# Kernel tuning notes

Hardware: AMD Instinct MI355X
Metric: run time of the kernel (lower is better)

The kernel has to match this reference:

```python
import jax, jax.numpy as jnp
import numpy as np

K_MASK = -2.3819763e+38

B, T, D = 2, 2048, 2048
N_HEADS, N_KV, HEAD_DIM = 16, 8, 128
SCALAR = 0.08838834764831845  # head_dim ** -0.5
ROPE_BASE = 10000


def rms_norm(x, scale):
    # fp32 mean-of-squares, rsqrt, bf16 round-trip, then scale (as in QwemmaRMSNorm)
    x32 = x.astype(jnp.float32)
    var = jnp.mean(jnp.square(x32), axis=-1, keepdims=True)
    rescaled = (x32 * jax.lax.rsqrt(var + 1e-06)).astype(jnp.bfloat16)
    return rescaled * scale


def apply_rope(inputs, positions, base_frequency):
    head_dim = inputs.shape[-1]
    fraction = 2 * jnp.arange(0, head_dim // 2) / head_dim
    timescale = base_frequency ** fraction
    sinusoid = positions[..., jnp.newaxis] / timescale[jnp.newaxis, jnp.newaxis, :]
    sinusoid = sinusoid[..., jnp.newaxis, :]  # [B,T,1,H/2]
    sin = jnp.sin(sinusoid).astype(inputs.dtype)
    cos = jnp.cos(sinusoid).astype(inputs.dtype)
    first, second = jnp.split(inputs, 2, axis=-1)
    out = jnp.concatenate([first * cos - second * sin,
                           second * cos + first * sin], axis=-1)
    return out.astype(inputs.dtype)


def setup_inputs() -> dict:
    key = jax.random.key(0)
    ks = jax.random.split(key, 7)
    x = jax.random.normal(ks[0], (B, T, D), dtype=jnp.float32)
    segment_pos = jnp.broadcast_to(jnp.arange(T, dtype=jnp.int32)[None, :], (B, T))
    attn_mask = jnp.broadcast_to(jnp.tril(jnp.ones((T, T), dtype=bool))[None], (B, T, T))
    q_w = jax.random.normal(ks[1], (N_HEADS, D, HEAD_DIM), dtype=jnp.float32) * 0.02
    kv_w = jax.random.normal(ks[2], (2, N_KV, D, HEAD_DIM), dtype=jnp.float32) * 0.02
    o_w = jax.random.normal(ks[3], (N_HEADS, HEAD_DIM, D), dtype=jnp.float32) * 0.02
    q_scale = 1.0 + 0.1 * jax.random.normal(ks[4], (HEAD_DIM,), dtype=jnp.float32)
    k_scale = 1.0 + 0.1 * jax.random.normal(ks[5], (HEAD_DIM,), dtype=jnp.float32)
    return {"x": x, "segment_pos": segment_pos, "attn_mask": attn_mask,
            "q_w": q_w, "kv_w": kv_w, "o_w": o_w,
            "q_scale": q_scale, "k_scale": k_scale}


def reference(x, segment_pos, attn_mask, q_w, kv_w, o_w, q_scale, k_scale):
    # projections
    q = jnp.einsum('BTD,NDH->BTNH', x, q_w)
    k, v = jnp.einsum('BSD,CKDH->CBSKH', x, kv_w)
    # QK RMSNorm + RoPE
    q = apply_rope(rms_norm(q, q_scale), segment_pos, ROPE_BASE)
    k = apply_rope(rms_norm(k, k_scale), segment_pos, ROPE_BASE)
    # GQA: [B,T,N,H] -> [B,T,K,G,H]
    b, t, n, h = q.shape
    g = n // N_KV
    q = q.reshape((b, t, N_KV, g, h))
    logits = jnp.einsum('BTKGH,BSKH->BTKGS', q, k)
    logits = (logits.astype(jnp.float32) * SCALAR).astype(jnp.bfloat16)
    s = logits.shape[-1]
    logits = logits.reshape((b, t, n, s))
    padded = jnp.where(jnp.expand_dims(attn_mask, -2), logits, K_MASK)
    probs = jax.nn.softmax(padded.astype(jnp.float32), axis=-1).astype(k.dtype)
    probs = probs.reshape((b, t, N_KV, g, s))
    encoded = jnp.einsum('BTKGS,BSKH->BTKGH', probs, v)
    encoded = encoded.reshape((b, t, n, h))
    return jnp.einsum('BTNH,NHD->BTD', encoded, o_w)


if __name__ == '__main__':
    out = reference(**setup_inputs())
    print(out.shape, out.dtype)
```

## Files before the change

kernel.cpp:

```cpp
#include <hip/hip_runtime.h>

typedef unsigned short u16;
typedef __attribute__((ext_vector_type(4))) float f32x4;
typedef __attribute__((ext_vector_type(8))) short s16x8;

#define SCALAR_F 0.08838834764831845f
#define KMASKF (-1e30f)

__device__ __forceinline__ u16 f2b(float f){
  unsigned u = __float_as_uint(f);
  unsigned r = u + 0x7FFFu + ((u>>16)&1u);
  return (u16)(r>>16);
}
__device__ __forceinline__ float b2f(u16 h){ return __uint_as_float(((unsigned)h)<<16); }

__device__ __forceinline__ f32x4 mfma16(s16x8 a, s16x8 b, f32x4 c){
  return __builtin_amdgcn_mfma_f32_16x16x32_bf16(a, b, c, 0, 0, 0);
}

__device__ __forceinline__ void glds16(const u16* g, u16* l){
  __builtin_amdgcn_global_load_lds((const __attribute__((address_space(1))) unsigned*)g,
                                   (__attribute__((address_space(3))) unsigned*)l, 16, 0, 0);
}

#define PHASE_BAR() asm volatile("s_barrier" ::: "memory")
#define LGKM0()     do { asm volatile("s_waitcnt lgkmcnt(0)" ::: "memory"); __builtin_amdgcn_sched_barrier(0); } while(0)

__global__ __launch_bounds__(256) void cvt_f32_bf16(const float* __restrict__ in, u16* __restrict__ out){
  int i = blockIdx.x*256 + threadIdx.x;
  const float4* p = (const float4*)in;
  float4 a = p[2*i], b = p[2*i+1];
  s16x8 r;
  r[0]=(short)f2b(a.x); r[1]=(short)f2b(a.y); r[2]=(short)f2b(a.z); r[3]=(short)f2b(a.w);
  r[4]=(short)f2b(b.x); r[5]=(short)f2b(b.y); r[6]=(short)f2b(b.z); r[7]=(short)f2b(b.w);
  *(s16x8*)(out + (size_t)i*8) = r;
}

__global__ __launch_bounds__(256) void build_wqkvt(const float* __restrict__ qw, const float* __restrict__ kvw,
                                                   u16* __restrict__ out){
  __shared__ float t[64][65];
  int head = blockIdx.z;
  int d0 = blockIdx.y*64, h0 = blockIdx.x*64;
  const float* src; int colbase;
  if (head < 16){ src = qw + (size_t)head*2048*128; colbase = head*128; }
  else if (head < 24){ int k = head-16; src = kvw + (size_t)k*2048*128; colbase = 2048 + k*128; }
  else { int k = head-24; src = kvw + (size_t)(8+k)*2048*128; colbase = 3072 + k*128; }
  int tid = threadIdx.x;
  #pragma unroll
  for (int p=0;p<16;p++){ int e = p*256+tid; int r = e>>6, c = e&63;
    t[r][c] = src[(size_t)(d0+r)*128 + h0 + c]; }
  __syncthreads();
  #pragma unroll
  for (int p=0;p<16;p++){ int e = p*256+tid; int c = e>>6, r = e&63;
    out[(size_t)(colbase + h0 + c)*2048 + d0 + r] = f2b(t[r][c]); }
}

__global__ __launch_bounds__(256) void tr2048(const float* __restrict__ src, u16* __restrict__ out){
  __shared__ float t[64][65];
  int r0 = blockIdx.y*64, c0 = blockIdx.x*64;
  int tid = threadIdx.x;
  #pragma unroll
  for (int p=0;p<16;p++){ int e = p*256+tid; int r = e>>6, c = e&63;
    t[r][c] = src[(size_t)(r0+r)*2048 + c0 + c]; }
  __syncthreads();
  #pragma unroll
  for (int p=0;p<16;p++){ int e = p*256+tid; int c = e>>6, r = e&63;
    out[(size_t)(c0+c)*2048 + r0 + r] = f2b(t[r][c]); }
}

__global__ __launch_bounds__(256) void rope_table(float* __restrict__ table){
  int tid = blockIdx.x*256 + threadIdx.x;
  int pos = tid>>6, i = tid&63;
  float ts = powf(10000.f, (float)i * (1.f/64.f));
  float ang = (float)pos / ts;
  ((float2*)table)[tid] = make_float2(sinf(ang), cosf(ang));
}

__global__ __launch_bounds__(512,2) void gemm256(const u16* __restrict__ A, const u16* __restrict__ Bt,
                                                 u16* __restrict__ C, int K, int ldc){
  __shared__ u16 Als[2][2][128*64];
  __shared__ u16 Bls[2][2][128*64];
  const int tid = threadIdx.x;
  const int wid = tid>>6, l = tid&63;
  const int wr = wid>>2, wc = wid&3;
  const int l15 = l&15, lg = l>>4;
  const int wg = blockIdx.x;
  const int swz = (wg&7)*32 + (wg>>3);
  const size_t m0 = (size_t)(swz>>4)*256, n0 = (size_t)(swz&15)*256;

  const f32x4 z4 = {0.f,0.f,0.f,0.f};
  f32x4 acc[8][4];
  #pragma unroll
  for (int mi=0;mi<8;mi++)
    #pragma unroll
    for (int ni=0;ni<4;ni++) acc[mi][ni] = z4;

  auto stageA = [&](int k0, int bi, int h){
    #pragma unroll
    for (int c=0;c<2;c++){
      int g = c*512 + tid;
      int row = g>>3, pg = g&7;
      glds16(A + (m0 + h*128 + row)*K + k0 + ((pg ^ (row&7))<<3), &Als[bi][h][0] + g*8);
    }
  };
  auto stageB = [&](int k0, int bi, int h){
    #pragma unroll
    for (int c=0;c<2;c++){
      int g = c*512 + tid;
      int row = g>>3, pg = g&7;
      glds16(Bt + (n0 + h*128 + row)*K + k0 + ((pg ^ (row&7))<<3), &Bls[bi][h][0] + g*8);
    }
  };

  s16x8 af[8][2], bf[4][2];

  const int NT = K>>6;
  stageA(0,0,0); stageA(0,0,1); stageB(0,0,0); stageB(0,0,1);
  stageA(64,1,0); stageA(64,1,1);
  asm volatile("s_waitcnt vmcnt(4)" ::: "memory");
  PHASE_BAR();

  for (int t=0; t<NT; ++t){
    const int bi = t&1;
    const char* Ab = (const char*)&Als[bi][wr][0];
    const char* Bb = (const char*)&Bls[bi][wc>>1][0];
    const int brl = (wc&1)*64;
    const int kn1 = (t+1)<<6, kn2 = (t+2)<<6;

    #pragma unroll
    for (int mi=0;mi<4;mi++){
      int r = mi*16 + l15;
      #pragma unroll
      for (int kk=0;kk<2;kk++)
        af[mi][kk] = *(const s16x8*)(Ab + r*128 + (((kk*4+lg) ^ (r&7))<<4));
    }
    #pragma unroll
    for (int ni=0;ni<2;ni++){
      int r = brl + ni*16 + l15;
      #pragma unroll
      for (int kk=0;kk<2;kk++)
        bf[ni][kk] = *(const s16x8*)(Bb + r*128 + (((kk*4+lg) ^ (r&7))<<4));
    }
    if (t+1 < NT) stageB(kn1, bi^1, 0);
    PHASE_BAR(); LGKM0();
    __builtin_amdgcn_s_setprio(1);
    #pragma unroll
    for (int mi=0;mi<4;mi++)
      #pragma unroll
      for (int ni=0;ni<2;ni++)
        #pragma unroll
        for (int kk=0;kk<2;kk++)
          acc[mi][ni] = mfma16(af[mi][kk], bf[ni][kk], acc[mi][ni]);
    __builtin_amdgcn_s_setprio(0);
    PHASE_BAR();

    #pragma unroll
    for (int ni=2;ni<4;ni++){
      int r = brl + ni*16 + l15;
      #pragma unroll
      for (int kk=0;kk<2;kk++)
        bf[ni][kk] = *(const s16x8*)(Bb + r*128 + (((kk*4+lg) ^ (r&7))<<4));
    }
    if (t+1 < NT) stageB(kn1, bi^1, 1);
    PHASE_BAR(); LGKM0();
    __builtin_amdgcn_s_setprio(1);
    #pragma unroll
    for (int mi=0;mi<4;mi++)
      #pragma unroll
      for (int ni=2;ni<4;ni++)
        #pragma unroll
        for (int kk=0;kk<2;kk++)
          acc[mi][ni] = mfma16(af[mi][kk], bf[ni][kk], acc[mi][ni]);
    __builtin_amdgcn_s_setprio(0);
    PHASE_BAR();

    #pragma unroll
    for (int mi=4;mi<8;mi++){
      int r = mi*16 + l15;
      #pragma unroll
      for (int kk=0;kk<2;kk++)
        af[mi][kk] = *(const s16x8*)(Ab + r*128 + (((kk*4+lg) ^ (r&7))<<4));
    }
    PHASE_BAR(); LGKM0();
    __builtin_amdgcn_s_setprio(1);
    #pragma unroll
    for (int mi=4;mi<8;mi++)
      #pragma unroll
      for (int ni=2;ni<4;ni++)
        #pragma unroll
        for (int kk=0;kk<2;kk++)
          acc[mi][ni] = mfma16(af[mi][kk], bf[ni][kk], acc[mi][ni]);
    __builtin_amdgcn_s_setprio(0);
    PHASE_BAR();

    if (t+2 < NT){ stageA(kn2, bi, 0); stageA(kn2, bi, 1); }
    __builtin_amdgcn_s_setprio(1);
    #pragma unroll
    for (int mi=4;mi<8;mi++)
      #pragma unroll
      for (int ni=0;ni<2;ni++)
        #pragma unroll
        for (int kk=0;kk<2;kk++)
          acc[mi][ni] = mfma16(af[mi][kk], bf[ni][kk], acc[mi][ni]);
    __builtin_amdgcn_s_setprio(0);
    if (t < NT-2)      { asm volatile("s_waitcnt vmcnt(4)" ::: "memory"); }
    else if (t == NT-2){ asm volatile("s_waitcnt vmcnt(0)" ::: "memory"); }
    PHASE_BAR();
  }

  #pragma unroll
  for (int mi=0;mi<8;mi++)
    #pragma unroll
    for (int ni=0;ni<4;ni++)
      #pragma unroll
      for (int r=0;r<4;r++){
        size_t row = m0 + wr*128 + mi*16 + lg*4 + r;
        size_t col = n0 + wc*64 + ni*16 + l15;
        C[row*ldc + col] = f2b(acc[mi][ni][r]);
      }
}

template<bool OUTBF16>
__global__ __launch_bounds__(256) void gemm_bt(const u16* __restrict__ A, const u16* __restrict__ Bt,
                                               void* __restrict__ C, int K, int ldc){
  __shared__ u16 As[128*64];
  __shared__ u16 Bs[128*64];
  const int tid = threadIdx.x, w = tid>>6, l = tid&63;
  const int wm = w>>1, wn = w&1;
  const int l15 = l&15, lg = l>>4, l7 = l&7;
  const size_t m0 = (size_t)blockIdx.y*128, n0 = (size_t)blockIdx.x*128;
  const f32x4 z4 = {0.f,0.f,0.f,0.f};
  f32x4 acc[4][4];
  #pragma unroll
  for (int m=0;m<4;m++)
    #pragma unroll
    for (int n=0;n<4;n++) acc[m][n] = z4;
  const char* AsB = (const char*)As; const char* BsB = (const char*)Bs;
  int colsw[2];
  colsw[0] = (lg*16) ^ (l7<<4);
  colsw[1] = (64 + lg*16) ^ (l7<<4);
  int arow[4], brow[4];
  #pragma unroll
  for (int m=0;m<4;m++){ arow[m] = (wm*64 + m*16 + l15)*128; brow[m] = (wn*64 + m*16 + l15)*128; }
  const int sgl = l7 ^ (l>>3);
  for (int k0=0;k0<K;k0+=64){
    #pragma unroll
    for (int i=0;i<4;i++){
      int slot = (w*4+i)*64 + l;
      int row = slot>>3;
      glds16(A  + (m0+row)*K + k0 + sgl*8, (u16*)As + slot*8);
      glds16(Bt + (n0+row)*K + k0 + sgl*8, (u16*)Bs + slot*8);
    }
    __syncthreads();
    #pragma unroll
    for (int kb=0;kb<2;kb++){
      s16x8 af[4], bf[4];
      #pragma unroll
      for (int m=0;m<4;m++) af[m] = *(const s16x8*)(AsB + arow[m] + colsw[kb]);
      #pragma unroll
      for (int n=0;n<4;n++) bf[n] = *(const s16x8*)(BsB + brow[n] + colsw[kb]);
      #pragma unroll
      for (int m=0;m<4;m++)
        #pragma unroll
        for (int n=0;n<4;n++)
          acc[m][n] = mfma16(af[m], bf[n], acc[m][n]);
    }
    __syncthreads();
  }
  #pragma unroll
  for (int m=0;m<4;m++)
    #pragma unroll
    for (int n=0;n<4;n++)
      #pragma unroll
      for (int r=0;r<4;r++){
        size_t row = m0 + wm*64 + m*16 + lg*4 + r;
        size_t col = n0 + wn*64 + n*16 + l15;
        if (OUTBF16) ((u16*)C)[row*ldc + col] = f2b(acc[m][n][r]);
        else ((float*)C)[row*ldc + col] = acc[m][n][r];
      }
}

__global__ __launch_bounds__(256) void norm_rope(const u16* __restrict__ qkv, const float* __restrict__ table,
                                                 const float* __restrict__ scale, const int* __restrict__ segpos,
                                                 u16* __restrict__ dst, int nhl2, int colbase, float mult){
  int w = threadIdx.x>>6, l = threadIdx.x&63;
  int rid = blockIdx.x*4 + w;
  int bt = rid >> nhl2;
  int n  = rid & ((1<<nhl2)-1);
  int b = bt >> 11, t = bt & 2047;
  const u16* src = qkv + (size_t)bt*4096 + colbase + n*128;
  float x1 = b2f(src[l]), x2 = b2f(src[64+l]);
  float ss = x1*x1 + x2*x2;
  #pragma unroll
  for (int off=32; off; off>>=1) ss += __shfl_xor(ss, off);
  float rs = rsqrtf(ss*(1.f/128.f) + 1e-6f);
  float v1 = x1*rs*scale[l], v2 = x2*rs*scale[64+l];
  int pos = segpos[bt];
  float2 sc = ((const float2*)table)[pos*64 + l];
  float o1 = (v1*sc.y - v2*sc.x)*mult;
  float o2 = (v2*sc.y + v1*sc.x)*mult;
  u16* d = dst + (((size_t)((b<<nhl2) + n))*2048 + t)*128;
  d[l] = f2b(o1); d[64+l] = f2b(o2);
}

__global__ __launch_bounds__(256) void vtr(const u16* __restrict__ qkv, u16* __restrict__ vt){
  __shared__ float t[64][65];
  int bk = blockIdx.z;
  int t0 = blockIdx.y*64, d0 = blockIdx.x*64;
  int b = bk>>3, kv = bk&7;
  int tid = threadIdx.x;
  #pragma unroll
  for (int p=0;p<16;p++){ int e = p*256+tid; int r = e>>6, c = e&63;
    t[r][c] = b2f(qkv[(size_t)(b*2048 + t0 + r)*4096 + 3072 + kv*128 + d0 + c]); }
  __syncthreads();
  #pragma unroll
  for (int p=0;p<16;p++){ int e = p*256+tid; int c = e>>6, r = e&63;
    vt[((size_t)bk*128 + d0 + c)*2048 + t0 + r] = f2b(t[r][c]); }
}

__global__ __launch_bounds__(256,2) void attn_kern(const u16* __restrict__ qn, const u16* __restrict__ kn,
                                                   const u16* __restrict__ vt, u16* __restrict__ enc){
  __shared__ u16 Ks[2][64*128];
  __shared__ u16 Vs[2][64*128];
  __shared__ u16 Ps[4*16*64];
  const int idx = blockIdx.x;
  const int pp = idx>>5;
  const int hb = idx & 31;
  const int hn = hb & 15, b = hb >> 4;
  const int kv = hn>>1;
  const int tid = threadIdx.x, w = tid>>6, l = tid&63;
  const int l15 = l&15, lg = l>>4;
  const u16* qh = qn + ((size_t)(b*16+hn))*2048*128;
  const u16* kh = kn + ((size_t)(b*8+kv))*2048*128;
  const u16* vh = vt + ((size_t)(b*8+kv))*128*2048;
  const int qbA = pp, qbB = 31-pp;

  int qr0 = qbA*64 + w*16;
  s16x8 qf[4];
  #pragma unroll
  for (int kb=0;kb<4;kb++)
    qf[kb] = *(const s16x8*)(qh + (size_t)(qr0 + l15)*128 + kb*32 + lg*8);

  const f32x4 z4 = {0.f,0.f,0.f,0.f};
  f32x4 o[8];
  #pragma unroll
  for (int dn=0;dn<8;dn++) o[dn] = z4;
  float mrow[4], lp[4];
  #pragma unroll
  for (int r=0;r<4;r++){ mrow[r] = KMASKF; lp[r] = 0.f; }

  const char* KsB0 = (const char*)&Ks[0][0];
  const char* VsB0 = (const char*)&Vs[0][0];
  char* PsB = (char*)Ps + w*2048;

  auto stage = [&](int s0, int bi){
    #pragma unroll
    for (int i=0;i<4;i++){
      int slot = (w*4+i)*64 + l;
      { int row = slot>>4, g = slot&15, gl = g ^ (row&7);
        glds16(kh + (size_t)(s0+row)*128 + gl*8, &Ks[bi][0] + slot*8); }
      { int row = slot>>3, g = slot&7, gl = g ^ (row&7);
        glds16(vh + (size_t)row*2048 + s0 + gl*8, &Vs[bi][0] + slot*8); }
    }
  };

  auto epilogue = [&](int qr){
    #pragma unroll
    for (int r=0;r<4;r++){
      float s = lp[r];
      s += __shfl_xor(s,1); s += __shfl_xor(s,2); s += __shfl_xor(s,4); s += __shfl_xor(s,8);
      lp[r] = 1.f/s;
    }
    #pragma unroll
    for (int dn=0;dn<8;dn++)
      #pragma unroll
      for (int r=0;r<4;r++){
        size_t row = (size_t)b*2048 + qr + lg*4 + r;
        size_t col = hn*128 + dn*16 + l15;
        enc[row*2048 + col] = f2b(o[dn][r]*lp[r]);
      }
  };

  stage(0, 0);
  __syncthreads();

  int cur = 0;
  for (int it=0; it<=32; ++it){
    if (it < 32){
      int s0n = (it+1 <= pp) ? (it+1)*64 : (it-pp)*64;
      stage(s0n, cur^1);
    }
    const int s0 = (it <= pp) ? it*64 : (it-pp-1)*64;
    const char* KsB = KsB0 + cur*16384;
    const char* VsB = VsB0 + cur*16384;

    f32x4 sa[4];
    #pragma unroll
    for (int nc=0;nc<4;nc++) sa[nc] = z4;
    #pragma unroll
    for (int kb=0;kb<4;kb++){
      s16x8 kf[4];
      #pragma unroll
      for (int nc=0;nc<4;nc++){
        int srow = nc*16 + l15;
        int cb = (kb*64 + lg*16) ^ ((srow&7)<<4);
        kf[nc] = *(const s16x8*)(KsB + srow*256 + cb);
      }
      #pragma unroll
      for (int nc=0;nc<4;nc++)
        sa[nc] = mfma16(qf[kb], kf[nc], sa[nc]);
    }
    if (it == pp || it == 32){
      #pragma unroll
      for (int nc=0;nc<4;nc++)
        #pragma unroll
        for (int r=0;r<4;r++){
          int row = qr0 + lg*4 + r;
          int col = s0 + nc*16 + l15;
          if (col > row) sa[nc][r] = KMASKF;
        }
    }
    #pragma unroll
    for (int r=0;r<4;r++){
      float pm = fmaxf(fmaxf(sa[0][r], sa[1][r]), fmaxf(sa[2][r], sa[3][r]));
      pm = fmaxf(pm, __shfl_xor(pm,1));
      pm = fmaxf(pm, __shfl_xor(pm,2));
      pm = fmaxf(pm, __shfl_xor(pm,4));
      pm = fmaxf(pm, __shfl_xor(pm,8));
      float mo = mrow[r];
      float mn = fmaxf(mo, pm);
      float sc = __expf(mo - mn);
      mrow[r] = mn;
      int rowp = lg*4 + r;
      float ls = 0.f;
      #pragma unroll
      for (int nc=0;nc<4;nc++){
        float p = __expf(sa[nc][r] - mn);
        ls += p;
        int cb = ((nc*16 + l15)*2) ^ ((rowp&7)<<4);
        *(u16*)(PsB + rowp*128 + cb) = f2b(p);
      }
      lp[r] = lp[r]*sc + ls;
      #pragma unroll
      for (int dn=0;dn<8;dn++) o[dn][r] *= sc;
    }
    asm volatile("" ::: "memory");
    #pragma unroll
    for (int kb=0;kb<2;kb++){
      int rowp = l15;
      int cbp = (kb*64 + lg*16) ^ ((rowp&7)<<4);
      s16x8 pf = *(const s16x8*)(PsB + rowp*128 + cbp);
      #pragma unroll
      for (int dn=0;dn<8;dn++){
        int vrow = dn*16 + l15;
        int cb = (kb*64 + lg*16) ^ ((vrow&7)<<4);
        s16x8 vf = *(const s16x8*)(VsB + vrow*128 + cb);
        o[dn] = mfma16(pf, vf, o[dn]);
      }
    }
    if (it == pp){
      epilogue(qr0);
      qr0 = qbB*64 + w*16;
      #pragma unroll
      for (int kb=0;kb<4;kb++)
        qf[kb] = *(const s16x8*)(qh + (size_t)(qr0 + l15)*128 + kb*32 + lg*8);
      #pragma unroll
      for (int dn=0;dn<8;dn++) o[dn] = z4;
      #pragma unroll
      for (int r=0;r<4;r++){ mrow[r] = KMASKF; lp[r] = 0.f; }
    }
    __syncthreads();
    cur ^= 1;
  }
  epilogue(qr0);
}

extern "C" void kernel_launch(void* const* d_in, const int* in_sizes, int n_in,
                              void* d_out, int out_size, void* d_ws, size_t ws_size,
                              hipStream_t stream){
  const float* x      = (const float*)d_in[0];
  const int*   segpos = (const int*)d_in[1];
  const float* qw     = (const float*)d_in[3];
  const float* kvw    = (const float*)d_in[4];
  const float* ow     = (const float*)d_in[5];
  const float* qs     = (const float*)d_in[6];
  const float* ks     = (const float*)d_in[7];
  float* out = (float*)d_out;

  char* ws = (char*)d_ws;
  size_t off = 0;
  auto alloc = [&](size_t bytes)->void*{ void* p = ws + off; off += (bytes + 255) & ~(size_t)255; return p; };
  u16*   xb    = (u16*)alloc((size_t)4096*2048*2);
  u16*   wqkvt = (u16*)alloc((size_t)4096*2048*2);
  u16*   wot   = (u16*)alloc((size_t)2048*2048*2);
  u16*   qkv   = (u16*)alloc((size_t)4096*4096*2);
  u16*   qn    = (u16*)alloc((size_t)2*16*2048*128*2);
  u16*   kn    = (u16*)alloc((size_t)2*8*2048*128*2);
  u16*   vt    = (u16*)alloc((size_t)2*8*128*2048*2);
  u16*   enc   = (u16*)alloc((size_t)4096*2048*2);
  float* table = (float*)alloc((size_t)2048*64*2*4);

  cvt_f32_bf16<<<4096,256,0,stream>>>(x, xb);
  build_wqkvt<<<dim3(2,32,32),256,0,stream>>>(qw, kvw, wqkvt);
  tr2048<<<dim3(32,32),256,0,stream>>>(ow, wot);
  rope_table<<<512,256,0,stream>>>(table);
  gemm256<<<256,512,0,stream>>>(xb, wqkvt, qkv, 2048, 4096);
  norm_rope<<<16384,256,0,stream>>>(qkv, table, qs, segpos, qn, 4, 0,    SCALAR_F);
  norm_rope<<<8192, 256,0,stream>>>(qkv, table, ks, segpos, kn, 3, 2048, 1.0f);
  vtr<<<dim3(2,32,16),256,0,stream>>>(qkv, vt);
  attn_kern<<<512,256,0,stream>>>(qn, kn, vt, enc);
  gemm_bt<false><<<dim3(16,32),256,0,stream>>>(enc, wot, out, 2048, 2048);
}
```

Before: 358.6 us.

## Pipeline output GEMM, load V from global directly, lazy softmax rescale

Replaces the simple output-projection GEMM with a 512-thread, 256x128-tile kernel. It double-buffers K-tiles through LDS, uses a swizzled block order, splits MFMA phases with priority hints, and hides loads behind vmcnt waits. In attention, V tiles are no longer staged through LDS; each lane reads its V fragments straight from global memory, which frees LDS so occupancy can rise to 3 blocks per CU. The online softmax now skips the rescale unless the running max grows by more than 8 in some lane. This saves exp and multiply work, but uncoalesced global V reads and the looser max bound could cost performance or precision.

```diff
diff --git a/kernel.cpp b/kernel.cpp
--- a/kernel.cpp
+++ b/kernel.cpp
@@ -220,63 +220,135 @@
       }
 }
 
-template<bool OUTBF16>
-__global__ __launch_bounds__(256) void gemm_bt(const u16* __restrict__ A, const u16* __restrict__ Bt,
-                                               void* __restrict__ C, int K, int ldc){
-  __shared__ u16 As[128*64];
-  __shared__ u16 Bs[128*64];
-  const int tid = threadIdx.x, w = tid>>6, l = tid&63;
-  const int wm = w>>1, wn = w&1;
-  const int l15 = l&15, lg = l>>4, l7 = l&7;
-  const size_t m0 = (size_t)blockIdx.y*128, n0 = (size_t)blockIdx.x*128;
+__global__ __launch_bounds__(512,1) void gemm_o(const u16* __restrict__ A, const u16* __restrict__ Bt,
+                                                float* __restrict__ C, int K, int ldc){
+  __shared__ u16 Als[2][2][128*64];
+  __shared__ u16 Bls[2][128*64];
+  const int tid = threadIdx.x;
+  const int wid = tid>>6, l = tid&63;
+  const int wr = wid>>1, wc = wid&1;
+  const int l15 = l&15, lg = l>>4;
+  const int wg = blockIdx.x;
+  const int swz = (wg&7)*32 + (wg>>3);
+  const size_t m0 = (size_t)(swz>>4)*256, n0 = (size_t)(swz&15)*128;
+
   const f32x4 z4 = {0.f,0.f,0.f,0.f};
   f32x4 acc[4][4];
   #pragma unroll
-  for (int m=0;m<4;m++)
-    #pragma unroll
-    for (int n=0;n<4;n++) acc[m][n] = z4;
-  const char* AsB = (const char*)As; const char* BsB = (const char*)Bs;
-  int colsw[2];
-  colsw[0] = (lg*16) ^ (l7<<4);
-  colsw[1] = (64 + lg*16) ^ (l7<<4);
-  int arow[4], brow[4];
-  #pragma unroll
-  for (int m=0;m<4;m++){ arow[m] = (wm*64 + m*16 + l15)*128; brow[m] = (wn*64 + m*16 + l15)*128; }
-  const int sgl = l7 ^ (l>>3);
-  for (int k0=0;k0<K;k0+=64){
-    #pragma unroll
-    for (int i=0;i<4;i++){
-      int slot = (w*4+i)*64 + l;
-      int row = slot>>3;
-      glds16(A  + (m0+row)*K + k0 + sgl*8, (u16*)As + slot*8);
-      glds16(Bt + (n0+row)*K + k0 + sgl*8, (u16*)Bs + slot*8);
-    }
-    __syncthreads();
-    #pragma unroll
-    for (int kb=0;kb<2;kb++){
-      s16x8 af[4], bf[4];
-      #pragma unroll
-      for (int m=0;m<4;m++) af[m] = *(const s16x8*)(AsB + arow[m] + colsw[kb]);
-      #pragma unroll
-      for (int n=0;n<4;n++) bf[n] = *(const s16x8*)(BsB + brow[n] + colsw[kb]);
-      #pragma unroll
-      for (int m=0;m<4;m++)
-        #pragma unroll
-        for (int n=0;n<4;n++)
-          acc[m][n] = mfma16(af[m], bf[n], acc[m][n]);
-    }
-    __syncthreads();
+  for (int mi=0;mi<4;mi++)
+    #pragma unroll
+    for (int ni=0;ni<4;ni++) acc[mi][ni] = z4;
+
+  auto stageA = [&](int k0, int bi, int h){
+    #pragma unroll
+    for (int c=0;c<2;c++){
+      int g = c*512 + tid;
+      int row = g>>3, pg = g&7;
+      glds16(A + (m0 + h*128 + row)*K + k0 + ((pg ^ (row&7))<<3), &Als[bi][h][0] + g*8);
+    }
+  };
+  auto stageB = [&](int k0, int bi){
+    #pragma unroll
+    for (int c=0;c<2;c++){
+      int g = c*512 + tid;
+      int row = g>>3, pg = g&7;
+      glds16(Bt + (n0 + row)*K + k0 + ((pg ^ (row&7))<<3), &Bls[bi][0] + g*8);
+    }
+  };
+
+  s16x8 af[4][2], bf[4][2];
+
+  const int NT = K>>6;
+  stageA(0,0,0); stageA(0,0,1); stageB(0,0);
+  stageA(64,1,0); stageA(64,1,1);
+  asm volatile("s_waitcnt vmcnt(4)" ::: "memory");
+  PHASE_BAR();
+
+  for (int t=0; t<NT; ++t){
+    const int bi = t&1;
+    const char* Ab = (const char*)&Als[bi][wr>>1][0];
+    const char* Bb = (const char*)&Bls[bi][0];
+    const int arl = (wr&1)*64;
+    const int brl = wc*64;
+    const int kn1 = (t+1)<<6, kn2 = (t+2)<<6;
+
+    #pragma unroll
+    for (int mi=0;mi<2;mi++){
+      int r = arl + mi*16 + l15;
+      #pragma unroll
+      for (int kk=0;kk<2;kk++)
+        af[mi][kk] = *(const s16x8*)(Ab + r*128 + (((kk*4+lg) ^ (r&7))<<4));
+    }
+    #pragma unroll
+    for (int ni=0;ni<2;ni++){
+      int r = brl + ni*16 + l15;
+      #pragma unroll
+      for (int kk=0;kk<2;kk++)
+        bf[ni][kk] = *(const s16x8*)(Bb + r*128 + (((kk*4+lg) ^ (r&7))<<4));
+    }
+    if (t+1 < NT) stageB(kn1, bi^1);
+    PHASE_BAR(); LGKM0();
+    __builtin_amdgcn_s_setprio(1);
+    #pragma unroll
+    for (int mi=0;mi<2;mi++)
+      #pragma unroll
+      for (int ni=0;ni<2;ni++)
+        #pragma unroll
+        for (int kk=0;kk<2;kk++)
+          acc[mi][ni] = mfma16(af[mi][kk], bf[ni][kk], acc[mi][ni]);
+    __builtin_amdgcn_s_setprio(0);
+    PHASE_BAR();
+
+    #pragma unroll
+    for (int mi=2;mi<4;mi++){
+      int r = arl + mi*16 + l15;
+      #pragma unroll
+      for (int kk=0;kk<2;kk++)
+        af[mi][kk] = *(const s16x8*)(Ab + r*128 + (((kk*4+lg) ^ (r&7))<<4));
+    }
+    #pragma unroll
+    for (int ni=2;ni<4;ni++){
+      int r = brl + ni*16 + l15;
+      #pragma unroll
+      for (int kk=0;kk<2;kk++)
+        bf[ni][kk] = *(const s16x8*)(Bb + r*128 + (((kk*4+lg) ^ (r&7))<<4));
+    }
+    PHASE_BAR(); LGKM0();
+    __builtin_amdgcn_s_setprio(1);
+    #pragma unroll
+    for (int mi=0;mi<2;mi++)
+      #pragma unroll
+      for (int ni=2;ni<4;ni++)
+        #pragma unroll
+        for (int kk=0;kk<2;kk++)
+          acc[mi][ni] = mfma16(af[mi][kk], bf[ni][kk], acc[mi][ni]);
+    __builtin_amdgcn_s_setprio(0);
+    PHASE_BAR();
+
+    if (t+2 < NT){ stageA(kn2, bi, 0); stageA(kn2, bi, 1); }
+    __builtin_amdgcn_s_setprio(1);
+    #pragma unroll
+    for (int mi=2;mi<4;mi++)
+      #pragma unroll
+      for (int ni=0;ni<4;ni++)
+        #pragma unroll
+        for (int kk=0;kk<2;kk++)
+          acc[mi][ni] = mfma16(af[mi][kk], bf[ni][kk], acc[mi][ni]);
+    __builtin_amdgcn_s_setprio(0);
+    if (t < NT-2)      { asm volatile("s_waitcnt vmcnt(4)" ::: "memory"); }
+    else if (t == NT-2){ asm volatile("s_waitcnt vmcnt(0)" ::: "memory"); }
+    PHASE_BAR();
   }
-  #pragma unroll
-  for (int m=0;m<4;m++)
-    #pragma unroll
-    for (int n=0;n<4;n++)
+
+  #pragma unroll
+  for (int mi=0;mi<4;mi++)
+    #pragma unroll
+    for (int ni=0;ni<4;ni++)
       #pragma unroll
       for (int r=0;r<4;r++){
-        size_t row = m0 + wm*64 + m*16 + lg*4 + r;
-        size_t col = n0 + wn*64 + n*16 + l15;
-        if (OUTBF16) ((u16*)C)[row*ldc + col] = f2b(acc[m][n][r]);
-        else ((float*)C)[row*ldc + col] = acc[m][n][r];
+        size_t row = m0 + wr*64 + mi*16 + lg*4 + r;
+        size_t col = n0 + wc*64 + ni*16 + l15;
+        C[row*ldc + col] = acc[mi][ni][r];
       }
 }
 
@@ -318,10 +390,9 @@
     vt[((size_t)bk*128 + d0 + c)*2048 + t0 + r] = f2b(t[r][c]); }
 }
 
-__global__ __launch_bounds__(256,2) void attn_kern(const u16* __restrict__ qn, const u16* __restrict__ kn,
+__global__ __launch_bounds__(256,3) void attn_kern(const u16* __restrict__ qn, const u16* __restrict__ kn,
                                                    const u16* __restrict__ vt, u16* __restrict__ enc){
   __shared__ u16 Ks[2][64*128];
-  __shared__ u16 Vs[2][64*128];
   __shared__ u16 Ps[4*16*64];
   const int idx = blockIdx.x;
   const int pp = idx>>5;
@@ -350,17 +421,14 @@
   for (int r=0;r<4;r++){ mrow[r] = KMASKF; lp[r] = 0.f; }
 
   const char* KsB0 = (const char*)&Ks[0][0];
-  const char* VsB0 = (const char*)&Vs[0][0];
   char* PsB = (char*)Ps + w*2048;
 
   auto stage = [&](int s0, int bi){
     #pragma unroll
     for (int i=0;i<4;i++){
       int slot = (w*4+i)*64 + l;
-      { int row = slot>>4, g = slot&15, gl = g ^ (row&7);
-        glds16(kh + (size_t)(s0+row)*128 + gl*8, &Ks[bi][0] + slot*8); }
-      { int row = slot>>3, g = slot&7, gl = g ^ (row&7);
-        glds16(vh + (size_t)row*2048 + s0 + gl*8, &Vs[bi][0] + slot*8); }
+      int row = slot>>4, g = slot&15, gl = g ^ (row&7);
+      glds16(kh + (size_t)(s0+row)*128 + gl*8, &Ks[bi][0] + slot*8);
     }
   };
 
@@ -392,7 +460,6 @@
     }
     const int s0 = (it <= pp) ? it*64 : (it-pp-1)*64;
     const char* KsB = KsB0 + cur*16384;
-    const char* VsB = VsB0 + cur*16384;
 
     f32x4 sa[4];
     #pragma unroll
@@ -410,6 +477,12 @@
       for (int nc=0;nc<4;nc++)
         sa[nc] = mfma16(qf[kb], kf[nc], sa[nc]);
     }
+
+    s16x8 vfr[8];
+    #pragma unroll
+    for (int dn=0;dn<8;dn++)
+      vfr[dn] = *(const s16x8*)(vh + (size_t)(dn*16 + l15)*2048 + s0 + lg*8);
+
     if (it == pp || it == 32){
       #pragma unroll
       for (int nc=0;nc<4;nc++)
@@ -428,9 +501,15 @@
       pm = fmaxf(pm, __shfl_xor(pm,4));
       pm = fmaxf(pm, __shfl_xor(pm,8));
       float mo = mrow[r];
-      float mn = fmaxf(mo, pm);
-      float sc = __expf(mo - mn);
-      mrow[r] = mn;
+      float mn = mo;
+      if (!__all(pm <= mo + 8.f)){
+        mn = fmaxf(mo, pm);
+        float sc = __expf(mo - mn);
+        mrow[r] = mn;
+        lp[r] *= sc;
+        #pragma unroll
+        for (int dn=0;dn<8;dn++) o[dn][r] *= sc;
+      }
       int rowp = lg*4 + r;
       float ls = 0.f;
       #pragma unroll
@@ -440,9 +519,7 @@
         int cb = ((nc*16 + l15)*2) ^ ((rowp&7)<<4);
         *(u16*)(PsB + rowp*128 + cb) = f2b(p);
       }
-      lp[r] = lp[r]*sc + ls;
-      #pragma unroll
-      for (int dn=0;dn<8;dn++) o[dn][r] *= sc;
+      lp[r] += ls;
     }
     asm volatile("" ::: "memory");
     #pragma unroll
@@ -452,9 +529,8 @@
       s16x8 pf = *(const s16x8*)(PsB + rowp*128 + cbp);
       #pragma unroll
       for (int dn=0;dn<8;dn++){
-        int vrow = dn*16 + l15;
-        int cb = (kb*64 + lg*16) ^ ((vrow&7)<<4);
-        s16x8 vf = *(const s16x8*)(VsB + vrow*128 + cb);
+        s16x8 vf = (kb==0) ? vfr[dn]
+                 : *(const s16x8*)(vh + (size_t)(dn*16 + l15)*2048 + s0 + 32 + lg*8);
         o[dn] = mfma16(pf, vf, o[dn]);
       }
     }
@@ -509,5 +585,5 @@
   norm_rope<<<8192, 256,0,stream>>>(qkv, table, ks, segpos, kn, 3, 2048, 1.0f);
   vtr<<<dim3(2,32,16),256,0,stream>>>(qkv, vt);
   attn_kern<<<512,256,0,stream>>>(qn, kn, vt, enc);
-  gemm_bt<false><<<dim3(16,32),256,0,stream>>>(enc, wot, out, 2048, 2048);
-}
+  gemm_o<<<256,512,0,stream>>>(enc, wot, out, 2048, 2048);
+}
```

After: 463.6 us. +29.3%, slower.
